# Kernel optimization log

Measured on AMD Instinct MI355X. Metric: run time of the kernel, lower is better.

Reference implementation:

```python
import jax, jax.numpy as jnp
import numpy as np
import math

N, M_ = 8192, 8192
QDIM, KDIM, MID = 512, 512, 256
SCALE = math.sqrt(MID)
NEG = -float(1 << 32)


def setup_inputs() -> dict:
    key = jax.random.key(0)
    ks = jax.random.split(key, 8)
    main_feat = jax.random.normal(ks[0], (N, QDIM), dtype=jnp.float32)
    other_feat = jax.random.normal(ks[1], (M_, KDIM), dtype=jnp.float32)
    fix_feat = jax.random.uniform(ks[2], (M_,), dtype=jnp.float32)
    mask = jax.random.randint(ks[3], (N, M_), 0, 2).astype(bool)
    # nn.Linear params (PyTorch layout: weight [out, in], bias [out])
    lim_q = 1.0 / math.sqrt(QDIM)
    lim_k = 1.0 / math.sqrt(KDIM)
    Wq = jax.random.uniform(ks[4], (MID, QDIM), minval=-lim_q, maxval=lim_q, dtype=jnp.float32)
    bq = jax.random.uniform(ks[5], (MID,), minval=-lim_q, maxval=lim_q, dtype=jnp.float32)
    Wk = jax.random.uniform(ks[6], (MID, KDIM), minval=-lim_k, maxval=lim_k, dtype=jnp.float32)
    bk = jax.random.uniform(ks[7], (MID,), minval=-lim_k, maxval=lim_k, dtype=jnp.float32)
    return {"main_feat": main_feat, "other_feat": other_feat, "fix_feat": fix_feat,
            "mask": mask, "Wq": Wq, "bq": bq, "Wk": Wk, "bk": bk}


def reference(main_feat, other_feat, fix_feat, mask, Wq, bq, Wk, bk):
    Q = main_feat @ Wq.T + bq                      # [N, MID]
    K = other_feat @ Wk.T + bk                     # [M, MID]
    A = jnp.einsum('nd,md->nm', Q, K) / SCALE      # [N, M]
    A = jnp.where(mask, jnp.float32(NEG), A)
    A = jax.nn.softmax(A, axis=-1)
    # diag(fix_feat) @ other_feat == row-wise scaling (no O(M^2) diag matrix)
    V = fix_feat[:, None] * other_feat             # [M, KDIM]
    return A @ V                                   # [N, KDIM]
```

## Files before the change

### kernel.cpp

```cpp
#include <hip/hip_runtime.h>
#include <stdint.h>


typedef short short8 __attribute__((ext_vector_type(8)));
typedef float f32x4 __attribute__((ext_vector_type(4)));

#define N_ROWS 8192
#define M_COLS 8192
#define QK_DIM 512
#define MID_D  256
#define OUT_D  512

__device__ __forceinline__ unsigned short f2b(float f) {
  union { float f; unsigned u; } x; x.f = f;
  unsigned r = x.u + 0x7FFFu + ((x.u >> 16) & 1u);
  return (unsigned short)(r >> 16);
}
__device__ __forceinline__ float b2f(unsigned short b) {
  union { unsigned u; float f; } x; x.u = ((unsigned)b) << 16;
  return x.f;
}

__device__ __forceinline__ f32x4 mfma16(short8 a, short8 b, f32x4 c) {
  return __builtin_amdgcn_mfma_f32_16x16x32_bf16(a, b, c, 0, 0, 0);
}

__device__ __forceinline__ void gload_lds16(const void* g, void* l) {
  __builtin_amdgcn_global_load_lds(
      (const __attribute__((address_space(1))) unsigned int*)g,
      (__attribute__((address_space(3))) unsigned int*)l, 16, 0, 0);
}

__global__ void detect_mask(const unsigned int* __restrict__ mask32,
                            int* __restrict__ params) {
  __shared__ int s_gt1, s_nzoff;
  if (threadIdx.x == 0) { s_gt1 = 0; s_nzoff = 0; }
  __syncthreads();
  int gt1 = 0, nz = 0;
  for (int i = threadIdx.x; i < 16384; i += 256) {
    unsigned w = mask32[i];
    #pragma unroll
    for (int k = 0; k < 4; ++k) {
      unsigned b = (w >> (8 * k)) & 0xFFu;
      if (b > 1) gt1 = 1;
      if (k && b) nz = 1;
    }
  }
  if (gt1) atomicOr(&s_gt1, 1);
  if (nz) atomicOr(&s_nzoff, 1);
  __syncthreads();
  if (threadIdx.x == 0) {
    int stride, off;
    if (s_gt1)        { stride = 4; off = 3; }
    else if (s_nzoff) { stride = 1; off = 0; }
    else              { stride = 4; off = 0; }
    params[0] = stride; params[1] = off;
  }
}

__global__ void prep_w(const float* __restrict__ Wq, const float* __restrict__ Wk,
                       unsigned short* __restrict__ Wqb, unsigned short* __restrict__ Wkb) {
  int b = blockIdx.x;
  const float* src = (b < 64) ? Wq : Wk;
  unsigned short* dst = (b < 64) ? Wqb : Wkb;
  int off = ((b & 63) * 256 + threadIdx.x) * 8;
  float4 v0 = *(const float4*)(src + off);
  float4 v1 = *(const float4*)(src + off + 4);
  alignas(16) unsigned short o[8] = {f2b(v0.x), f2b(v0.y), f2b(v0.z), f2b(v0.w),
                                     f2b(v1.x), f2b(v1.y), f2b(v1.z), f2b(v1.w)};
  *(short8*)(dst + off) = *(const short8*)o;
}

__global__ void prep_vt(const float* __restrict__ other, const float* __restrict__ fix,
                        unsigned short* __restrict__ Vt) {
  __shared__ unsigned short T[64][72];
  int m0 = blockIdx.x * 64, j0 = blockIdx.y * 64;
  int t = threadIdx.x;
  {
    int mr = t >> 2, jc = (t & 3) * 16;
    float f = fix[m0 + mr];
    const float* src = other + (size_t)(m0 + mr) * QK_DIM + j0 + jc;
    #pragma unroll
    for (int i = 0; i < 16; i += 4) {
      float4 v = *(const float4*)(src + i);
      T[mr][jc + i + 0] = f2b(v.x * f);
      T[mr][jc + i + 1] = f2b(v.y * f);
      T[mr][jc + i + 2] = f2b(v.z * f);
      T[mr][jc + i + 3] = f2b(v.w * f);
    }
  }
  __syncthreads();
  {
    int jr = t >> 2, mc = (t & 3) * 16;
    alignas(16) unsigned short o[16];
    #pragma unroll
    for (int i = 0; i < 16; ++i) o[i] = T[mc + i][jr];
    unsigned short* dst = Vt + (size_t)(j0 + jr) * M_COLS + m0 + mc;
    *(short8*)dst       = *(const short8*)o;
    *(short8*)(dst + 8) = *(const short8*)(o + 8);
  }
}

__global__ __launch_bounds__(256, 2) void proj_kernel(
    const float* __restrict__ X, const unsigned short* __restrict__ Wb,
    const float* __restrict__ bias, unsigned short* __restrict__ Out) {
  int lane = threadIdx.x & 63, wv = threadIdx.x >> 6;
  int l15 = lane & 15, l4 = lane >> 4;
  int rows0 = (blockIdx.x >> 1) * 64 + wv * 16;
  int ch = (blockIdx.x & 1) * 128;
  const float* xrow = X + (size_t)(rows0 + l15) * QK_DIM + l4 * 8;
  f32x4 acc[8];
  #pragma unroll
  for (int cg = 0; cg < 8; ++cg) acc[cg] = (f32x4){0.f, 0.f, 0.f, 0.f};
  for (int kk = 0; kk < 16; ++kk) {
    float4 a0 = *(const float4*)(xrow + kk * 32);
    float4 a1 = *(const float4*)(xrow + kk * 32 + 4);
    alignas(16) unsigned short ab[8] = {f2b(a0.x), f2b(a0.y), f2b(a0.z), f2b(a0.w),
                                        f2b(a1.x), f2b(a1.y), f2b(a1.z), f2b(a1.w)};
    short8 a = *(const short8*)ab;
    const unsigned short* wb = Wb + (size_t)(ch + l15) * QK_DIM + kk * 32 + l4 * 8;
    #pragma unroll
    for (int cg = 0; cg < 8; ++cg) {
      short8 b = *(const short8*)(wb + (size_t)cg * 16 * QK_DIM);
      acc[cg] = mfma16(a, b, acc[cg]);
    }
  }
  #pragma unroll
  for (int cg = 0; cg < 8; ++cg) {
    int j = ch + cg * 16 + l15;
    float bj = bias[j];
    #pragma unroll
    for (int r = 0; r < 4; ++r) {
      int row = rows0 + l4 * 4 + r;
      Out[(size_t)row * MID_D + j] = f2b(acc[cg][r] + bj);
    }
  }
}

__global__ __launch_bounds__(1024, 4) void fused_kernel(
    const unsigned short* __restrict__ Qb, const unsigned short* __restrict__ Kb,
    const unsigned short* __restrict__ Vt, const unsigned char* __restrict__ mask,
    const int* __restrict__ mparams, float* __restrict__ Op,
    float* __restrict__ rsp, int msLog, int kvlen) {
  __shared__ unsigned short Klds[64 * 256];
  __shared__ unsigned short Plds[64 * 64];
  __shared__ float rs_lds[4][64];

  const int tid = threadIdx.x;
  const int lane = tid & 63, wv = tid >> 6;
  const int l15 = lane & 15, l4 = lane >> 4;
  const int rg = wv >> 2, mg = wv & 3;
  const int ms = blockIdx.x & ((1 << msLog) - 1);
  const int rb = blockIdx.x >> msLog;
  const int n0 = rb * 64;
  const int kv0 = ms * kvlen;

  const size_t mstride = (size_t)mparams[0];
  const size_t moff = (size_t)mparams[1];

  short8 qf[8];
  {
    const unsigned short* q = Qb + (size_t)(n0 + rg * 16 + l15) * MID_D + l4 * 8;
    #pragma unroll
    for (int kk = 0; kk < 8; ++kk) qf[kk] = *(const short8*)(q + kk * 32);
  }

  f32x4 O[4][2];
  #pragma unroll
  for (int g = 0; g < 4; ++g)
    #pragma unroll
    for (int c = 0; c < 2; ++c) O[g][c] = (f32x4){0.f, 0.f, 0.f, 0.f};
  float rs[4] = {0.f, 0.f, 0.f, 0.f};

  const unsigned char* mbase =
      mask + ((size_t)(n0 + rg * 16 + l4 * 4) * M_COLS + kv0 + mg * 16 + l15) * mstride + moff;
  const unsigned short* kvK = Kb + (size_t)kv0 * MID_D;
  const unsigned short* kvV = Vt + kv0;

  for (int m0 = 0; m0 < kvlen; m0 += 64) {
    #pragma unroll
    for (int i = 0; i < 2; ++i) {
      int c = i * 1024 + tid;
      int m = c >> 5, d16 = c & 31;
      gload_lds16(kvK + (size_t)(m0 + m) * MID_D + ((d16 ^ (m & 7)) << 3),
                  &Klds[(size_t)c * 8]);
    }
    unsigned int mk[4];
    #pragma unroll
    for (int r = 0; r < 4; ++r) mk[r] = mbase[((size_t)r * M_COLS + m0) * mstride];

    __syncthreads();

    f32x4 s = {0.f, 0.f, 0.f, 0.f};
    {
      int m = mg * 16 + l15;
      const char* kb = (const char*)Klds + m * 512;
      int sw = (m & 7) << 4;
      #pragma unroll
      for (int kk = 0; kk < 8; ++kk) {
        short8 b = *(const short8*)(kb + (((kk * 32 + l4 * 8) * 2) ^ sw));
        s = mfma16(qf[kk], b, s);
      }
    }
    #pragma unroll
    for (int r = 0; r < 4; ++r) {
      int n = rg * 16 + l4 * 4 + r;
      float e = mk[r] ? 0.f : __expf(s[r] * 0.0625f);
      unsigned short pb = f2b(e);
      rs[r] += b2f(pb);
      *(unsigned short*)((char*)Plds +
          ((n * 128 + (mg * 16 + l15) * 2) ^ ((n & 7) << 4))) = pb;
    }
    __syncthreads();

    #pragma unroll
    for (int mm = 0; mm < 2; ++mm) {
      int krel = mm * 32 + l4 * 8;
      short8 a[4];
      #pragma unroll
      for (int g = 0; g < 4; ++g) {
        int n = g * 16 + l15;
        a[g] = *(const short8*)((const char*)Plds + ((n * 128 + krel * 2) ^ ((n & 7) << 4)));
      }
      short8 b0 = *(const short8*)(kvV + (size_t)(wv * 32 + l15) * M_COLS + m0 + krel);
      short8 b1 = *(const short8*)(kvV + (size_t)(wv * 32 + 16 + l15) * M_COLS + m0 + krel);
      #pragma unroll
      for (int g = 0; g < 4; ++g) {
        O[g][0] = mfma16(a[g], b0, O[g][0]);
        O[g][1] = mfma16(a[g], b1, O[g][1]);
      }
    }
  }

  #pragma unroll
  for (int r = 0; r < 4; ++r) {
    float v = rs[r];
    v += __shfl_xor(v, 1); v += __shfl_xor(v, 2);
    v += __shfl_xor(v, 4); v += __shfl_xor(v, 8);
    rs[r] = v;
  }
  if (l15 == 0) {
    #pragma unroll
    for (int r = 0; r < 4; ++r) rs_lds[mg][rg * 16 + l4 * 4 + r] = rs[r];
  }
  __syncthreads();
  if (tid < 64) {
    float t = rs_lds[0][tid] + rs_lds[1][tid] + rs_lds[2][tid] + rs_lds[3][tid];
    rsp[(size_t)ms * N_ROWS + n0 + tid] = t;
  }

  float* ob = Op + (size_t)blockIdx.x * (64 * 512);
  #pragma unroll
  for (int g = 0; g < 4; ++g) {
    #pragma unroll
    for (int r = 0; r < 4; ++r) {
      float* row = ob + (size_t)(g * 16 + l4 * 4 + r) * 512 + wv * 32 + l15;
      row[0]  = O[g][0][r];
      row[16] = O[g][1][r];
    }
  }
}

__global__ void combine_kernel(const float* __restrict__ Op, const float* __restrict__ rsp,
                               float* __restrict__ out, int MS) {
  int gid = blockIdx.x * 256 + threadIdx.x;
  int n = gid >> 7;
  int j = (gid & 127) << 2;
  int rb = n >> 6, r = n & 63;
  float a0 = 0.f, a1 = 0.f, a2 = 0.f, a3 = 0.f, d = 0.f;
  for (int ms = 0; ms < MS; ++ms) {
    const float* p = Op + (((size_t)rb * MS + ms) * 64 + r) * 512 + j;
    float4 v = *(const float4*)p;
    a0 += v.x; a1 += v.y; a2 += v.z; a3 += v.w;
    d += rsp[(size_t)ms * N_ROWS + n];
  }
  float inv = 1.0f / d;
  float4 o; o.x = a0 * inv; o.y = a1 * inv; o.z = a2 * inv; o.w = a3 * inv;
  *(float4*)(out + (size_t)n * OUT_D + j) = o;
}

extern "C" void kernel_launch(void* const* d_in, const int* in_sizes, int n_in,
                              void* d_out, int out_size, void* d_ws, size_t ws_size,
                              hipStream_t stream) {
  const float* main_feat = (const float*)d_in[0];
  const float* other     = (const float*)d_in[1];
  const float* fix       = (const float*)d_in[2];
  const unsigned char* mask = (const unsigned char*)d_in[3];
  const float* Wq = (const float*)d_in[4];
  const float* bq = (const float*)d_in[5];
  const float* Wk = (const float*)d_in[6];
  const float* bk = (const float*)d_in[7];
  float* out = (float*)d_out;

  char* ws = (char*)d_ws;
  unsigned short* Qb  = (unsigned short*)(ws);
  unsigned short* Kb  = (unsigned short*)(ws + ((size_t)4 << 20));
  unsigned short* Vt  = (unsigned short*)(ws + ((size_t)8 << 20));
  unsigned short* Wqb = (unsigned short*)(ws + ((size_t)16 << 20));
  unsigned short* Wkb = (unsigned short*)(ws + ((size_t)16 << 20) + (256 << 10));
  int* mparams        = (int*)(ws + ((size_t)16 << 20) + (512 << 10));
  float* rsp          = (float*)(ws + ((size_t)16 << 20) + (768 << 10));
  float* OpWs         = (float*)(ws + ((size_t)17 << 20));

  int msLog; float* Op;
  size_t base = (size_t)17 << 20;
  if (ws_size >= base + ((size_t)64 << 20))      { msLog = 2; Op = OpWs; }
  else if (ws_size >= base + ((size_t)32 << 20)) { msLog = 1; Op = OpWs; }
  else                                           { msLog = 0; Op = out; }
  int MS = 1 << msLog;
  int kvlen = M_COLS >> msLog;

  detect_mask<<<1, 256, 0, stream>>>((const unsigned int*)mask, mparams);
  prep_w<<<128, 256, 0, stream>>>(Wq, Wk, Wqb, Wkb);
  prep_vt<<<dim3(128, 8), 256, 0, stream>>>(other, fix, Vt);
  proj_kernel<<<256, 256, 0, stream>>>(main_feat, Wqb, bq, Qb);
  proj_kernel<<<256, 256, 0, stream>>>(other, Wkb, bk, Kb);
  fused_kernel<<<128 * MS, 1024, 0, stream>>>(Qb, Kb, Vt, mask, mparams,
                                              Op, rsp, msLog, kvlen);
  combine_kernel<<<4096, 256, 0, stream>>>(Op, rsp, out, MS);
}
```

Measured before the change: 675.2 us.

## Prepack mask to bits, double-buffer K tiles, and shrink fused blocks to 32 rows

Adds a pre-pass that packs the byte mask into per-row bitmasks, so the fused kernel reads one 32-bit word per 32 tiles instead of one byte per element each tile. The fused kernel now double-buffers K tiles in LDS, prefetching the next tile while the current one is computed, and uses raw barriers in place of __syncthreads. Blocks shrink to 512 threads covering 32 rows, each wave taking 64 output columns, which doubles the grid. The cost is an extra mask-packing kernel over the full mask, more LDS per block for the second K buffer, and more V loads per wave.

After: 772.5 us. 1.14x slower.

```diff
diff --git a/kernel.cpp b/kernel.cpp
--- a/kernel.cpp
+++ b/kernel.cpp
@@ -56,6 +56,23 @@
     else              { stride = 4; off = 0; }
     params[0] = stride; params[1] = off;
   }
+}
+
+__global__ __launch_bounds__(256) void prep_maskbits(
+    const unsigned char* __restrict__ mask, const int* __restrict__ mparams,
+    unsigned int* __restrict__ bmS) {
+  int lane = threadIdx.x & 63, wv = threadIdx.x >> 6;
+  int task = blockIdx.x * 4 + wv;
+  int n = task >> 2, w = task & 3;
+  size_t mstride = (size_t)mparams[0];
+  size_t moff = (size_t)mparams[1];
+  const unsigned char* src =
+      mask + ((size_t)n * M_COLS + w * 2048 + lane) * mstride + moff;
+  unsigned bits = 0;
+  #pragma unroll
+  for (int s = 0; s < 32; ++s)
+    if (src[(size_t)s * 64 * mstride]) bits |= (1u << s);
+  bmS[((size_t)n * 4 + w) * 64 + lane] = bits;
 }
 
 __global__ void prep_w(const float* __restrict__ Wq, const float* __restrict__ Wk,
@@ -137,14 +154,13 @@
   }
 }
 
-__global__ __launch_bounds__(1024, 4) void fused_kernel(
+__global__ __launch_bounds__(512, 4) void fused_kernel(
     const unsigned short* __restrict__ Qb, const unsigned short* __restrict__ Kb,
-    const unsigned short* __restrict__ Vt, const unsigned char* __restrict__ mask,
-    const int* __restrict__ mparams, float* __restrict__ Op,
-    float* __restrict__ rsp, int msLog, int kvlen) {
-  __shared__ unsigned short Klds[64 * 256];
-  __shared__ unsigned short Plds[64 * 64];
-  __shared__ float rs_lds[4][64];
+    const unsigned short* __restrict__ Vt, const unsigned int* __restrict__ bmS,
+    float* __restrict__ Op, float* __restrict__ rsp, int msLog, int kvlen) {
+  __shared__ unsigned short Klds[2][64 * 256];
+  __shared__ unsigned short Plds[32 * 64];
+  __shared__ float rs_lds[4][32];
 
   const int tid = threadIdx.x;
   const int lane = tid & 63, wv = tid >> 6;
@@ -152,11 +168,9 @@
   const int rg = wv >> 2, mg = wv & 3;
   const int ms = blockIdx.x & ((1 << msLog) - 1);
   const int rb = blockIdx.x >> msLog;
-  const int n0 = rb * 64;
+  const int n0 = rb * 32;
   const int kv0 = ms * kvlen;
-
-  const size_t mstride = (size_t)mparams[0];
-  const size_t moff = (size_t)mparams[1];
+  const int nt = kvlen >> 6;
 
   short8 qf[8];
   {
@@ -165,71 +179,91 @@
     for (int kk = 0; kk < 8; ++kk) qf[kk] = *(const short8*)(q + kk * 32);
   }
 
-  f32x4 O[4][2];
-  #pragma unroll
-  for (int g = 0; g < 4; ++g)
-    #pragma unroll
-    for (int c = 0; c < 2; ++c) O[g][c] = (f32x4){0.f, 0.f, 0.f, 0.f};
+  f32x4 O[2][4];
+  #pragma unroll
+  for (int og = 0; og < 2; ++og)
+    #pragma unroll
+    for (int cg = 0; cg < 4; ++cg) O[og][cg] = (f32x4){0.f, 0.f, 0.f, 0.f};
   float rs[4] = {0.f, 0.f, 0.f, 0.f};
 
-  const unsigned char* mbase =
-      mask + ((size_t)(n0 + rg * 16 + l4 * 4) * M_COLS + kv0 + mg * 16 + l15) * mstride + moff;
+  const unsigned int* bmp =
+      bmS + (((size_t)(n0 + rg * 16 + l4 * 4) * 4) + (kv0 >> 11)) * 64 + (mg * 16 + l15);
+  unsigned mcur[4];
+
   const unsigned short* kvK = Kb + (size_t)kv0 * MID_D;
   const unsigned short* kvV = Vt + kv0;
 
-  for (int m0 = 0; m0 < kvlen; m0 += 64) {
-    #pragma unroll
-    for (int i = 0; i < 2; ++i) {
-      int c = i * 1024 + tid;
-      int m = c >> 5, d16 = c & 31;
-      gload_lds16(kvK + (size_t)(m0 + m) * MID_D + ((d16 ^ (m & 7)) << 3),
-                  &Klds[(size_t)c * 8]);
-    }
-    unsigned int mk[4];
-    #pragma unroll
-    for (int r = 0; r < 4; ++r) mk[r] = mbase[((size_t)r * M_COLS + m0) * mstride];
-
-    __syncthreads();
-
+  #pragma unroll
+  for (int i = 0; i < 4; ++i) {
+    int c = i * 512 + tid;
+    int m = c >> 5, d16 = c & 31;
+    gload_lds16(kvK + (size_t)m * MID_D + ((d16 ^ (m & 7)) << 3), &Klds[0][c * 8]);
+  }
+  __syncthreads();
+
+  for (int t = 0; t < nt; ++t) {
+    const int cur = t & 1;
+    if (t + 1 < nt) {
+      #pragma unroll
+      for (int i = 0; i < 4; ++i) {
+        int c = i * 512 + tid;
+        int m = c >> 5, d16 = c & 31;
+        gload_lds16(kvK + (size_t)(((t + 1) << 6) + m) * MID_D + ((d16 ^ (m & 7)) << 3),
+                    &Klds[cur ^ 1][c * 8]);
+      }
+    }
+    if ((t & 31) == 0) {
+      #pragma unroll
+      for (int r = 0; r < 4; ++r) mcur[r] = bmp[r * 256];
+      bmp += 64;
+    }
     f32x4 s = {0.f, 0.f, 0.f, 0.f};
     {
       int m = mg * 16 + l15;
-      const char* kb = (const char*)Klds + m * 512;
+      const char* kb = (const char*)Klds[cur] + m * 512;
       int sw = (m & 7) << 4;
       #pragma unroll
-      for (int kk = 0; kk < 8; ++kk) {
-        short8 b = *(const short8*)(kb + (((kk * 32 + l4 * 8) * 2) ^ sw));
-        s = mfma16(qf[kk], b, s);
-      }
-    }
+      for (int kk = 0; kk < 8; ++kk)
+        s = mfma16(qf[kk], *(const short8*)(kb + (((kk * 32 + l4 * 8) * 2) ^ sw)), s);
+    }
+    const int tb = t & 31;
     #pragma unroll
     for (int r = 0; r < 4; ++r) {
       int n = rg * 16 + l4 * 4 + r;
-      float e = mk[r] ? 0.f : __expf(s[r] * 0.0625f);
+      float e = ((mcur[r] >> tb) & 1u) ? 0.f : __expf(s[r] * 0.0625f);
       unsigned short pb = f2b(e);
       rs[r] += b2f(pb);
       *(unsigned short*)((char*)Plds +
           ((n * 128 + (mg * 16 + l15) * 2) ^ ((n & 7) << 4))) = pb;
     }
-    __syncthreads();
-
-    #pragma unroll
-    for (int mm = 0; mm < 2; ++mm) {
-      int krel = mm * 32 + l4 * 8;
-      short8 a[4];
-      #pragma unroll
-      for (int g = 0; g < 4; ++g) {
-        int n = g * 16 + l15;
-        a[g] = *(const short8*)((const char*)Plds + ((n * 128 + krel * 2) ^ ((n & 7) << 4)));
+    asm volatile("s_waitcnt lgkmcnt(0)" ::: "memory");
+    __builtin_amdgcn_sched_barrier(0);
+    __builtin_amdgcn_s_barrier();
+    __builtin_amdgcn_sched_barrier(0);
+    {
+      const int m0 = t << 6;
+      #pragma unroll
+      for (int mm = 0; mm < 2; ++mm) {
+        int krel = mm * 32 + l4 * 8;
+        const unsigned short* vb = kvV + (size_t)(wv * 64 + l15) * M_COLS + m0 + krel;
+        short8 b[4];
+        #pragma unroll
+        for (int cg = 0; cg < 4; ++cg)
+          b[cg] = *(const short8*)(vb + (size_t)cg * 16 * M_COLS);
+        short8 a0 = *(const short8*)((const char*)Plds +
+                    ((l15 * 128 + krel * 2) ^ ((l15 & 7) << 4)));
+        short8 a1 = *(const short8*)((const char*)Plds +
+                    (((16 + l15) * 128 + krel * 2) ^ ((l15 & 7) << 4)));
+        #pragma unroll
+        for (int cg = 0; cg < 4; ++cg) {
+          O[0][cg] = mfma16(a0, b[cg], O[0][cg]);
+          O[1][cg] = mfma16(a1, b[cg], O[1][cg]);
+        }
       }
-      short8 b0 = *(const short8*)(kvV + (size_t)(wv * 32 + l15) * M_COLS + m0 + krel);
-      short8 b1 = *(const short8*)(kvV + (size_t)(wv * 32 + 16 + l15) * M_COLS + m0 + krel);
-      #pragma unroll
-      for (int g = 0; g < 4; ++g) {
-        O[g][0] = mfma16(a[g], b0, O[g][0]);
-        O[g][1] = mfma16(a[g], b1, O[g][1]);
-      }
-    }
+    }
+    __builtin_amdgcn_sched_barrier(0);
+    __builtin_amdgcn_s_barrier();
+    __builtin_amdgcn_sched_barrier(0);
   }
 
   #pragma unroll
@@ -244,19 +278,19 @@
     for (int r = 0; r < 4; ++r) rs_lds[mg][rg * 16 + l4 * 4 + r] = rs[r];
   }
   __syncthreads();
-  if (tid < 64) {
-    float t = rs_lds[0][tid] + rs_lds[1][tid] + rs_lds[2][tid] + rs_lds[3][tid];
-    rsp[(size_t)ms * N_ROWS + n0 + tid] = t;
-  }
-
-  float* ob = Op + (size_t)blockIdx.x * (64 * 512);
-  #pragma unroll
-  for (int g = 0; g < 4; ++g) {
+  if (tid < 32) {
+    float tsum = rs_lds[0][tid] + rs_lds[1][tid] + rs_lds[2][tid] + rs_lds[3][tid];
+    rsp[(size_t)ms * N_ROWS + n0 + tid] = tsum;
+  }
+
+  float* ob = Op + (size_t)blockIdx.x * (32 * 512);
+  #pragma unroll
+  for (int og = 0; og < 2; ++og) {
     #pragma unroll
     for (int r = 0; r < 4; ++r) {
-      float* row = ob + (size_t)(g * 16 + l4 * 4 + r) * 512 + wv * 32 + l15;
-      row[0]  = O[g][0][r];
-      row[16] = O[g][1][r];
+      float* row = ob + (size_t)(og * 16 + l4 * 4 + r) * 512 + wv * 64 + l15;
+      #pragma unroll
+      for (int cg = 0; cg < 4; ++cg) row[cg * 16] = O[og][cg][r];
     }
   }
 }
@@ -266,10 +300,10 @@
   int gid = blockIdx.x * 256 + threadIdx.x;
   int n = gid >> 7;
   int j = (gid & 127) << 2;
-  int rb = n >> 6, r = n & 63;
+  int rb = n >> 5, r = n & 31;
   float a0 = 0.f, a1 = 0.f, a2 = 0.f, a3 = 0.f, d = 0.f;
   for (int ms = 0; ms < MS; ++ms) {
-    const float* p = Op + (((size_t)rb * MS + ms) * 64 + r) * 512 + j;
+    const float* p = Op + (((size_t)rb * MS + ms) * 32 + r) * 512 + j;
     float4 v = *(const float4*)p;
     a0 += v.x; a1 += v.y; a2 += v.z; a3 += v.w;
     d += rsp[(size_t)ms * N_ROWS + n];
@@ -296,14 +330,15 @@
   unsigned short* Qb  = (unsigned short*)(ws);
   unsigned short* Kb  = (unsigned short*)(ws + ((size_t)4 << 20));
   unsigned short* Vt  = (unsigned short*)(ws + ((size_t)8 << 20));
-  unsigned short* Wqb = (unsigned short*)(ws + ((size_t)16 << 20));
-  unsigned short* Wkb = (unsigned short*)(ws + ((size_t)16 << 20) + (256 << 10));
-  int* mparams        = (int*)(ws + ((size_t)16 << 20) + (512 << 10));
-  float* rsp          = (float*)(ws + ((size_t)16 << 20) + (768 << 10));
-  float* OpWs         = (float*)(ws + ((size_t)17 << 20));
+  unsigned int*  bmS  = (unsigned int*)(ws + ((size_t)16 << 20));
+  unsigned short* Wqb = (unsigned short*)(ws + ((size_t)24 << 20));
+  unsigned short* Wkb = (unsigned short*)(ws + ((size_t)24 << 20) + (256 << 10));
+  int* mparams        = (int*)(ws + ((size_t)24 << 20) + (512 << 10));
+  float* rsp          = (float*)(ws + ((size_t)24 << 20) + (768 << 10));
+  float* OpWs         = (float*)(ws + ((size_t)25 << 20));
 
   int msLog; float* Op;
-  size_t base = (size_t)17 << 20;
+  size_t base = (size_t)25 << 20;
   if (ws_size >= base + ((size_t)64 << 20))      { msLog = 2; Op = OpWs; }
   else if (ws_size >= base + ((size_t)32 << 20)) { msLog = 1; Op = OpWs; }
   else                                           { msLog = 0; Op = out; }
@@ -311,11 +346,11 @@
   int kvlen = M_COLS >> msLog;
 
   detect_mask<<<1, 256, 0, stream>>>((const unsigned int*)mask, mparams);
+  prep_maskbits<<<8192, 256, 0, stream>>>(mask, mparams, bmS);
   prep_w<<<128, 256, 0, stream>>>(Wq, Wk, Wqb, Wkb);
   prep_vt<<<dim3(128, 8), 256, 0, stream>>>(other, fix, Vt);
   proj_kernel<<<256, 256, 0, stream>>>(main_feat, Wqb, bq, Qb);
   proj_kernel<<<256, 256, 0, stream>>>(other, Wkb, bk, Kb);
-  fused_kernel<<<128 * MS, 1024, 0, stream>>>(Qb, Kb, Vt, mask, mparams,
-                                              Op, rsp, msLog, kvlen);
+  fused_kernel<<<256 * MS, 512, 0, stream>>>(Qb, Kb, Vt, bmS, Op, rsp, msLog, kvlen);
   combine_kernel<<<4096, 256, 0, stream>>>(Op, rsp, out, MS);
 }
```
